# Optimization experiments

Hardware: AMD Instinct MI355X
Metric: run time of the kernel (lower is better)

## Reference

```python
import jax, jax.numpy as jnp
import numpy as np

N_STREAMS = 4096


def setup_inputs() -> dict:
    key = jax.random.key(0)
    # Plain Gaussian (well-separated singular values; the polar factor math is
    # identical to the module's eye + 0.01*randn init, just a different point).
    H_raw = jax.random.normal(key, (N_STREAMS, N_STREAMS), dtype=jnp.float32)
    return {"H_raw": H_raw}


def reference(H_raw) -> jnp.ndarray:
    # OrthogonalMixing.forward: orthogonal polar factor of H_raw via thin SVD.
    U, s, Vh = jnp.linalg.svd(H_raw, full_matrices=False)
    return U @ Vh  # (s, s), satisfies H^T H = I
```

## Files before the change

kernel.cpp:

```cpp
#include <hip/hip_runtime.h>
#include <hip/hip_bf16.h>

#define NN 4096
#define NITER 12
#define NGROW 9
#define NPOW 12

using bf16 = __hip_bfloat16;
typedef __attribute__((ext_vector_type(4))) float f32x4;
typedef __attribute__((ext_vector_type(8))) short s16x8;
typedef __attribute__((ext_vector_type(8))) unsigned short u16x8;

__device__ inline float bf2f(unsigned short u) {
  union { unsigned int i; float f; } c; c.i = ((unsigned int)u) << 16; return c.f;
}
__device__ inline unsigned short f2bf(float f) {
  bf16 t = (bf16)f; return *(unsigned short*)&t;
}

__device__ inline void gl_lds16(const void* g, void* l) {
  __builtin_amdgcn_global_load_lds(
      (const __attribute__((address_space(1))) unsigned int*)(unsigned long long)(uintptr_t)g,
      (__attribute__((address_space(3))) unsigned int*)(uintptr_t)l,
      16, 0, 0);
}

template <int EPI, int TRI>
__global__ __launch_bounds__(256, 2) void gemm_nt(
    const bf16* __restrict__ P, const bf16* __restrict__ Q,
    void* __restrict__ Out, const bf16* __restrict__ aux,
    float alpha, float beta) {
  if (TRI && blockIdx.y > blockIdx.x) return;
  __shared__ bf16 lp[128 * 64];
  __shared__ bf16 lq[128 * 64];

  const int tid = threadIdx.x;
  const int lane = tid & 63;
  const int wv = tid >> 6;
  const int wr = wv >> 1, wc = wv & 1;
  const int bi = blockIdx.x, bj = blockIdx.y;

  const int m = lane & 15;
  const int qd = lane >> 4;
  const int lrow = lane >> 3;
  const int lchunk = lane & 7;

  f32x4 acc[4][4] = {};

  for (int k0 = 0; k0 < NN; k0 += 64) {
    __syncthreads();
#pragma unroll
    for (int s = 0; s < 4; ++s) {
      const int t = wv * 4 + s;
      const int r = t * 8 + lrow;
      const int gc = lchunk ^ (r & 7);
      const bf16* gp = P + (size_t)(bi * 128 + r) * NN + k0 + gc * 8;
      gl_lds16(gp, &lp[t * 512 + lane * 8]);
      const bf16* gq = Q + (size_t)(bj * 128 + r) * NN + k0 + gc * 8;
      gl_lds16(gq, &lq[t * 512 + lane * 8]);
    }
    __syncthreads();

#pragma unroll
    for (int sub = 0; sub < 2; ++sub) {
      s16x8 av[4], bv[4];
#pragma unroll
      for (int f = 0; f < 4; ++f) {
        const int ra = wr * 64 + f * 16 + m;
        const int ca = (sub * 4 + qd) ^ (ra & 7);
        av[f] = *(const s16x8*)&lp[ra * 64 + ca * 8];
        const int rb = wc * 64 + f * 16 + m;
        const int cb = (sub * 4 + qd) ^ (rb & 7);
        bv[f] = *(const s16x8*)&lq[rb * 64 + cb * 8];
      }
#pragma unroll
      for (int fr = 0; fr < 4; ++fr)
#pragma unroll
        for (int fc = 0; fc < 4; ++fc)
          acc[fr][fc] = __builtin_amdgcn_mfma_f32_16x16x32_bf16(
              av[fr], bv[fc], acc[fr][fc], 0, 0, 0);
    }
  }

#pragma unroll
  for (int fr = 0; fr < 4; ++fr) {
#pragma unroll
    for (int fc = 0; fc < 4; ++fc) {
#pragma unroll
      for (int rg = 0; rg < 4; ++rg) {
        const int grow = bi * 128 + wr * 64 + fr * 16 + qd * 4 + rg;
        const int gcol = bj * 128 + wc * 64 + fc * 16 + m;
        const size_t idx = (size_t)grow * NN + gcol;
        float v = beta * acc[fr][fc][rg];
        if (alpha != 0.0f) v += alpha * (float)aux[idx];
        if (EPI == 0)
          ((bf16*)Out)[idx] = (bf16)v;
        else
          ((float*)Out)[idx] = v;
      }
    }
  }
}

__global__ void transpose_bf16(const bf16* __restrict__ in, bf16* __restrict__ out) {
  __shared__ bf16 tile[64][65];
  const int tx = threadIdx.x & 63;
  const int ty = threadIdx.x >> 6;
  const int bx = blockIdx.x, by = blockIdx.y;
#pragma unroll
  for (int rr = 0; rr < 16; ++rr) {
    const int row = rr * 4 + ty;
    tile[row][tx] = in[(size_t)(by * 64 + row) * NN + bx * 64 + tx];
  }
  __syncthreads();
#pragma unroll
  for (int rr = 0; rr < 16; ++rr) {
    const int row = rr * 4 + ty;
    out[(size_t)(bx * 64 + row) * NN + by * 64 + tx] = tile[tx][row];
  }
}

__global__ void mirror_upper(bf16* __restrict__ A) {
  const int bx = blockIdx.x, by = blockIdx.y;
  if (by <= bx) return;
  __shared__ bf16 tile[64][65];
  const int tx = threadIdx.x & 63;
  const int ty = threadIdx.x >> 6;
#pragma unroll
  for (int rr = 0; rr < 16; ++rr) {
    const int row = rr * 4 + ty;
    tile[row][tx] = A[(size_t)(by * 64 + row) * NN + bx * 64 + tx];
  }
  __syncthreads();
#pragma unroll
  for (int rr = 0; rr < 16; ++rr) {
    const int row = rr * 4 + ty;
    A[(size_t)(bx * 64 + row) * NN + by * 64 + tx] = tile[tx][row];
  }
}

__global__ __launch_bounds__(256) void powmv(const bf16* __restrict__ A,
                                             const float* __restrict__ vin,
                                             const float* __restrict__ snin,
                                             float* __restrict__ vout,
                                             float* __restrict__ snout) {
  const float scale = rsqrtf(*snin);
  const int row = blockIdx.x * 4 + (threadIdx.x >> 6);
  const int lane = threadIdx.x & 63;
  const unsigned short* arow = (const unsigned short*)A + (size_t)row * NN;
  float acc = 0.0f;
#pragma unroll
  for (int p = 0; p < 8; ++p) {
    const int c = p * 512 + lane * 8;
    const u16x8 av = *(const u16x8*)(arow + c);
    const float4 w0 = *(const float4*)(vin + c);
    const float4 w1 = *(const float4*)(vin + c + 4);
    acc += bf2f(av[0]) * w0.x + bf2f(av[1]) * w0.y + bf2f(av[2]) * w0.z +
           bf2f(av[3]) * w0.w + bf2f(av[4]) * w1.x + bf2f(av[5]) * w1.y +
           bf2f(av[6]) * w1.z + bf2f(av[7]) * w1.w;
  }
  for (int off = 32; off; off >>= 1) acc += __shfl_down(acc, off, 64);
  if (lane == 0) {
    const float u = acc * scale;
    vout[row] = u;
    atomicAdd(snout, u * u);
  }
}

__global__ void init_pw(float* __restrict__ v0, float* __restrict__ slots) {
  const int t = threadIdx.x;
  if (t < 64) slots[t] = (t == 1) ? 1.0f : 0.0f;
  for (int i = t; i < NN; i += 256) {
    const unsigned h = (unsigned)i * 2654435761u;
    v0[i] = ((h >> 16) & 1) ? 0.015625f : -0.015625f;
  }
}

__global__ void reduce_sumsq(const float* __restrict__ h, float* __restrict__ slots) {
  float acc = 0.0f;
  const size_t total = (size_t)NN * NN;
  for (size_t i = (size_t)blockIdx.x * blockDim.x + threadIdx.x; i < total;
       i += (size_t)gridDim.x * blockDim.x) {
    const float v = h[i];
    acc += v * v;
  }
  for (int off = 32; off; off >>= 1) acc += __shfl_down(acc, off, 64);
  __shared__ float ws[4];
  const int lane = threadIdx.x & 63, wv = threadIdx.x >> 6;
  if (lane == 0) ws[wv] = acc;
  __syncthreads();
  if (threadIdx.x == 0) atomicAdd(&slots[0], ws[0] + ws[1] + ws[2] + ws[3]);
}

__global__ void scale_cast(const float* __restrict__ h, const float* __restrict__ slots,
                           bf16* __restrict__ xb, int mode) {
  float inv = rsqrtf(slots[0]);
  if (mode) inv *= rsqrtf(1.10f * sqrtf(slots[1 + NPOW]));
  const size_t i = ((size_t)blockIdx.x * blockDim.x + threadIdx.x) * 4;
  const float4 v = *(const float4*)(h + i);
  union { bf16 b[4]; ushort4 u; } cvt;
  cvt.b[0] = (bf16)(v.x * inv);
  cvt.b[1] = (bf16)(v.y * inv);
  cvt.b[2] = (bf16)(v.z * inv);
  cvt.b[3] = (bf16)(v.w * inv);
  *(ushort4*)(xb + i) = cvt.u;
}

__global__ void rescale_bf16(bf16* __restrict__ a, const float* __restrict__ slots) {
  const float cA = 1.0f / (1.10f * sqrtf(slots[1 + NPOW]));
  const size_t i = ((size_t)blockIdx.x * 256 + threadIdx.x) * 8;
  unsigned short* p = (unsigned short*)a + i;
  u16x8 v = *(u16x8*)p;
  u16x8 o;
#pragma unroll
  for (int j = 0; j < 8; ++j) o[j] = f2bf(bf2f(v[j]) * cA);
  *(u16x8*)p = o;
}

extern "C" void kernel_launch(void* const* d_in, const int* in_sizes, int n_in,
                              void* d_out, int out_size, void* d_ws, size_t ws_size,
                              hipStream_t stream) {
  (void)in_sizes; (void)n_in; (void)out_size; (void)ws_size;
  const float* H = (const float*)d_in[0];
  float* out = (float*)d_out;
  char* ws = (char*)d_ws;

  bf16* P0 = (bf16*)ws;
  bf16* P1 = (bf16*)(ws + ((size_t)32 << 20));
  bf16* Ab = (bf16*)(ws + ((size_t)64 << 20));
  bf16* Bb = (bf16*)((char*)d_out + ((size_t)32 << 20));
  float* v0 = (float*)d_out;
  float* v1 = (float*)((char*)d_out + 16384);
  float* slots = (float*)((char*)d_out + 32768);

  const dim3 g(32, 32), tb(256), gt(64, 64);

  init_pw<<<1, 256, 0, stream>>>(v0, slots);
  reduce_sumsq<<<1024, 256, 0, stream>>>(H, slots);
  scale_cast<<<(NN * (size_t)NN) / 4 / 256, 256, 0, stream>>>(H, slots, P0, 0);
  transpose_bf16<<<gt, tb, 0, stream>>>(P0, P1);
  gemm_nt<0, 1><<<g, tb, 0, stream>>>(P1, P1, Ab, (bf16*)nullptr, 0.0f, 1.0f);
  mirror_upper<<<gt, tb, 0, stream>>>(Ab);
  for (int k = 0; k < NPOW; ++k) {
    const float* vi = (k & 1) ? v1 : v0;
    float* vo = (k & 1) ? v0 : v1;
    powmv<<<1024, 256, 0, stream>>>(Ab, vi, &slots[1 + k], vo, &slots[2 + k]);
  }
  rescale_bf16<<<(NN * (size_t)NN) / 8 / 256, 256, 0, stream>>>(Ab, slots);
  scale_cast<<<(NN * (size_t)NN) / 4 / 256, 256, 0, stream>>>(H, slots, P0, 1);

  bf16* X = P0;
  bf16* Y = P1;
  const float GA = 3.4445f, GB = -4.7750f, GC = 2.0315f;
  const float PA = 1.875f, PB = -1.25f, PC = 0.375f;

  for (int it = 0; it < NITER; ++it) {
    const bool polish = it >= NGROW;
    const bool last = (it == NITER - 1);
    const float qa = polish ? PA : GA, qb = polish ? PB : GB, qc = polish ? PC : GC;

    if (it > 0) {
      transpose_bf16<<<gt, tb, 0, stream>>>(X, Y);
      gemm_nt<0, 1><<<g, tb, 0, stream>>>(Y, Y, Ab, (bf16*)nullptr, 0.0f, 1.0f);
      mirror_upper<<<gt, tb, 0, stream>>>(Ab);
    }
    bf16* Bdst = last ? Y : Bb;
    gemm_nt<0, 1><<<g, tb, 0, stream>>>(Ab, Ab, Bdst, Ab, qb, qc);
    mirror_upper<<<gt, tb, 0, stream>>>(Bdst);
    if (!last) {
      gemm_nt<0, 0><<<g, tb, 0, stream>>>(X, Bdst, Y, X, qa, 1.0f);
      bf16* t = X; X = Y; Y = t;
    } else {
      gemm_nt<1, 0><<<g, tb, 0, stream>>>(X, Bdst, out, X, qa, 1.0f);
    }
  }
}
```

Measured before the change: 5.321 ms.

## Switch polar iteration to fp16, packed triangular grid, fused mirroring, fewer iterations

Moves every matrix and the MFMA path from bf16 to fp16, with a prescale of 32 on X so values keep fp16 precision. Launches only the 528 lower-triangle tiles through a triangular index map and writes the mirrored tile from the GEMM epilogue, which removes the separate mirror kernels and the early-exit blocks. Cuts the Newton-Schulz schedule from 12 iterations to 10 (8 growth, 2 polish) and raises the launch-bounds occupancy hint. The fewer polish steps and the fp16 range both put accuracy at risk, and the scattered transposed stores in the epilogue are uncoalesced.

```diff
diff --git a/kernel.cpp b/kernel.cpp
--- a/kernel.cpp
+++ b/kernel.cpp
@@ -1,22 +1,18 @@
 #include <hip/hip_runtime.h>
 #include <hip/hip_bf16.h>
+#include <hip/hip_fp16.h>
 
 #define NN 4096
-#define NITER 12
-#define NGROW 9
+#define NGROW 8
+#define NPOL 2
+#define NITER (NGROW + NPOL)
 #define NPOW 12
-
-using bf16 = __hip_bfloat16;
+#define NTRI 528
+#define PRESCALE 32.0f
+
+using f16 = _Float16;
 typedef __attribute__((ext_vector_type(4))) float f32x4;
-typedef __attribute__((ext_vector_type(8))) short s16x8;
-typedef __attribute__((ext_vector_type(8))) unsigned short u16x8;
-
-__device__ inline float bf2f(unsigned short u) {
-  union { unsigned int i; float f; } c; c.i = ((unsigned int)u) << 16; return c.f;
-}
-__device__ inline unsigned short f2bf(float f) {
-  bf16 t = (bf16)f; return *(unsigned short*)&t;
-}
+typedef __attribute__((ext_vector_type(8))) f16 h16x8;
 
 __device__ inline void gl_lds16(const void* g, void* l) {
   __builtin_amdgcn_global_load_lds(
@@ -26,19 +22,30 @@
 }
 
 template <int EPI, int TRI>
-__global__ __launch_bounds__(256, 2) void gemm_nt(
-    const bf16* __restrict__ P, const bf16* __restrict__ Q,
-    void* __restrict__ Out, const bf16* __restrict__ aux,
+__global__ __launch_bounds__(256, 4) void gemm_nt(
+    const f16* __restrict__ P, const f16* __restrict__ Q,
+    void* __restrict__ Out, const f16* __restrict__ aux,
     float alpha, float beta) {
-  if (TRI && blockIdx.y > blockIdx.x) return;
-  __shared__ bf16 lp[128 * 64];
-  __shared__ bf16 lq[128 * 64];
+  int bi, bj;
+  if (TRI) {
+    const int t = blockIdx.x;
+    int r = (int)((sqrtf(8.0f * (float)t + 1.0f) - 1.0f) * 0.5f);
+    while ((r + 1) * (r + 2) / 2 <= t) ++r;
+    while (r * (r + 1) / 2 > t) --r;
+    bi = r;
+    bj = t - r * (r + 1) / 2;
+  } else {
+    bi = blockIdx.x;
+    bj = blockIdx.y;
+  }
+
+  __shared__ f16 lp[128 * 64];
+  __shared__ f16 lq[128 * 64];
 
   const int tid = threadIdx.x;
   const int lane = tid & 63;
   const int wv = tid >> 6;
   const int wr = wv >> 1, wc = wv & 1;
-  const int bi = blockIdx.x, bj = blockIdx.y;
 
   const int m = lane & 15;
   const int qd = lane >> 4;
@@ -54,30 +61,30 @@
       const int t = wv * 4 + s;
       const int r = t * 8 + lrow;
       const int gc = lchunk ^ (r & 7);
-      const bf16* gp = P + (size_t)(bi * 128 + r) * NN + k0 + gc * 8;
+      const f16* gp = P + (size_t)(bi * 128 + r) * NN + k0 + gc * 8;
       gl_lds16(gp, &lp[t * 512 + lane * 8]);
-      const bf16* gq = Q + (size_t)(bj * 128 + r) * NN + k0 + gc * 8;
+      const f16* gq = Q + (size_t)(bj * 128 + r) * NN + k0 + gc * 8;
       gl_lds16(gq, &lq[t * 512 + lane * 8]);
     }
     __syncthreads();
 
 #pragma unroll
     for (int sub = 0; sub < 2; ++sub) {
-      s16x8 av[4], bv[4];
+      h16x8 av[4], bv[4];
 #pragma unroll
       for (int f = 0; f < 4; ++f) {
         const int ra = wr * 64 + f * 16 + m;
         const int ca = (sub * 4 + qd) ^ (ra & 7);
-        av[f] = *(const s16x8*)&lp[ra * 64 + ca * 8];
+        av[f] = *(const h16x8*)&lp[ra * 64 + ca * 8];
         const int rb = wc * 64 + f * 16 + m;
         const int cb = (sub * 4 + qd) ^ (rb & 7);
-        bv[f] = *(const s16x8*)&lq[rb * 64 + cb * 8];
+        bv[f] = *(const h16x8*)&lq[rb * 64 + cb * 8];
       }
 #pragma unroll
       for (int fr = 0; fr < 4; ++fr)
 #pragma unroll
         for (int fc = 0; fc < 4; ++fc)
-          acc[fr][fc] = __builtin_amdgcn_mfma_f32_16x16x32_bf16(
+          acc[fr][fc] = __builtin_amdgcn_mfma_f32_16x16x32_f16(
               av[fr], bv[fc], acc[fr][fc], 0, 0, 0);
     }
   }
@@ -88,22 +95,27 @@
     for (int fc = 0; fc < 4; ++fc) {
 #pragma unroll
       for (int rg = 0; rg < 4; ++rg) {
-        const int grow = bi * 128 + wr * 64 + fr * 16 + qd * 4 + rg;
-        const int gcol = bj * 128 + wc * 64 + fc * 16 + m;
-        const size_t idx = (size_t)grow * NN + gcol;
+        const int lr = wr * 64 + fr * 16 + qd * 4 + rg;
+        const int lc = wc * 64 + fc * 16 + m;
+        const size_t idx = (size_t)(bi * 128 + lr) * NN + bj * 128 + lc;
         float v = beta * acc[fr][fc][rg];
         if (alpha != 0.0f) v += alpha * (float)aux[idx];
         if (EPI == 0)
-          ((bf16*)Out)[idx] = (bf16)v;
+          ((f16*)Out)[idx] = (f16)v;
         else
           ((float*)Out)[idx] = v;
+        if (TRI && bi != bj) {
+          const size_t idxT = (size_t)(bj * 128 + lc) * NN + bi * 128 + lr;
+          ((f16*)Out)[idxT] = (f16)v;
+        }
       }
     }
   }
 }
 
-__global__ void transpose_bf16(const bf16* __restrict__ in, bf16* __restrict__ out) {
-  __shared__ bf16 tile[64][65];
+__global__ void transpose_h(const unsigned short* __restrict__ in,
+                            unsigned short* __restrict__ out) {
+  __shared__ unsigned short tile[64][65];
   const int tx = threadIdx.x & 63;
   const int ty = threadIdx.x >> 6;
   const int bx = blockIdx.x, by = blockIdx.y;
@@ -120,26 +132,7 @@
   }
 }
 
-__global__ void mirror_upper(bf16* __restrict__ A) {
-  const int bx = blockIdx.x, by = blockIdx.y;
-  if (by <= bx) return;
-  __shared__ bf16 tile[64][65];
-  const int tx = threadIdx.x & 63;
-  const int ty = threadIdx.x >> 6;
-#pragma unroll
-  for (int rr = 0; rr < 16; ++rr) {
-    const int row = rr * 4 + ty;
-    tile[row][tx] = A[(size_t)(by * 64 + row) * NN + bx * 64 + tx];
-  }
-  __syncthreads();
-#pragma unroll
-  for (int rr = 0; rr < 16; ++rr) {
-    const int row = rr * 4 + ty;
-    A[(size_t)(bx * 64 + row) * NN + by * 64 + tx] = tile[tx][row];
-  }
-}
-
-__global__ __launch_bounds__(256) void powmv(const bf16* __restrict__ A,
+__global__ __launch_bounds__(256) void powmv(const f16* __restrict__ A,
                                              const float* __restrict__ vin,
                                              const float* __restrict__ snin,
                                              float* __restrict__ vout,
@@ -147,17 +140,17 @@
   const float scale = rsqrtf(*snin);
   const int row = blockIdx.x * 4 + (threadIdx.x >> 6);
   const int lane = threadIdx.x & 63;
-  const unsigned short* arow = (const unsigned short*)A + (size_t)row * NN;
+  const f16* arow = A + (size_t)row * NN;
   float acc = 0.0f;
 #pragma unroll
   for (int p = 0; p < 8; ++p) {
     const int c = p * 512 + lane * 8;
-    const u16x8 av = *(const u16x8*)(arow + c);
+    const h16x8 av = *(const h16x8*)(arow + c);
     const float4 w0 = *(const float4*)(vin + c);
     const float4 w1 = *(const float4*)(vin + c + 4);
-    acc += bf2f(av[0]) * w0.x + bf2f(av[1]) * w0.y + bf2f(av[2]) * w0.z +
-           bf2f(av[3]) * w0.w + bf2f(av[4]) * w1.x + bf2f(av[5]) * w1.y +
-           bf2f(av[6]) * w1.z + bf2f(av[7]) * w1.w;
+    acc += (float)av[0] * w0.x + (float)av[1] * w0.y + (float)av[2] * w0.z +
+           (float)av[3] * w0.w + (float)av[4] * w1.x + (float)av[5] * w1.y +
+           (float)av[6] * w1.z + (float)av[7] * w1.w;
   }
   for (int off = 32; off; off >>= 1) acc += __shfl_down(acc, off, 64);
   if (lane == 0) {
@@ -193,28 +186,27 @@
 }
 
 __global__ void scale_cast(const float* __restrict__ h, const float* __restrict__ slots,
-                           bf16* __restrict__ xb, int mode) {
-  float inv = rsqrtf(slots[0]);
+                           f16* __restrict__ xb, int mode) {
+  float inv = rsqrtf(slots[0]) * PRESCALE;
   if (mode) inv *= rsqrtf(1.10f * sqrtf(slots[1 + NPOW]));
   const size_t i = ((size_t)blockIdx.x * blockDim.x + threadIdx.x) * 4;
   const float4 v = *(const float4*)(h + i);
-  union { bf16 b[4]; ushort4 u; } cvt;
-  cvt.b[0] = (bf16)(v.x * inv);
-  cvt.b[1] = (bf16)(v.y * inv);
-  cvt.b[2] = (bf16)(v.z * inv);
-  cvt.b[3] = (bf16)(v.w * inv);
+  union { f16 hh[4]; ushort4 u; } cvt;
+  cvt.hh[0] = (f16)(v.x * inv);
+  cvt.hh[1] = (f16)(v.y * inv);
+  cvt.hh[2] = (f16)(v.z * inv);
+  cvt.hh[3] = (f16)(v.w * inv);
   *(ushort4*)(xb + i) = cvt.u;
 }
 
-__global__ void rescale_bf16(bf16* __restrict__ a, const float* __restrict__ slots) {
+__global__ void rescale_f16(f16* __restrict__ a, const float* __restrict__ slots) {
   const float cA = 1.0f / (1.10f * sqrtf(slots[1 + NPOW]));
   const size_t i = ((size_t)blockIdx.x * 256 + threadIdx.x) * 8;
-  unsigned short* p = (unsigned short*)a + i;
-  u16x8 v = *(u16x8*)p;
-  u16x8 o;
-#pragma unroll
-  for (int j = 0; j < 8; ++j) o[j] = f2bf(bf2f(v[j]) * cA);
-  *(u16x8*)p = o;
+  h16x8 v = *(h16x8*)(a + i);
+  h16x8 o;
+#pragma unroll
+  for (int j = 0; j < 8; ++j) o[j] = (f16)((float)v[j] * cA);
+  *(h16x8*)(a + i) = o;
 }
 
 extern "C" void kernel_launch(void* const* d_in, const int* in_sizes, int n_in,
@@ -225,32 +217,31 @@
   float* out = (float*)d_out;
   char* ws = (char*)d_ws;
 
-  bf16* P0 = (bf16*)ws;
-  bf16* P1 = (bf16*)(ws + ((size_t)32 << 20));
-  bf16* Ab = (bf16*)(ws + ((size_t)64 << 20));
-  bf16* Bb = (bf16*)((char*)d_out + ((size_t)32 << 20));
+  f16* P0 = (f16*)ws;
+  f16* P1 = (f16*)(ws + ((size_t)32 << 20));
+  f16* Ab = (f16*)(ws + ((size_t)64 << 20));
+  f16* Bb = (f16*)((char*)d_out + ((size_t)32 << 20));
   float* v0 = (float*)d_out;
   float* v1 = (float*)((char*)d_out + 16384);
   float* slots = (float*)((char*)d_out + 32768);
 
-  const dim3 g(32, 32), tb(256), gt(64, 64);
+  const dim3 gfull(32, 32), tb(256), gt(64, 64);
 
   init_pw<<<1, 256, 0, stream>>>(v0, slots);
   reduce_sumsq<<<1024, 256, 0, stream>>>(H, slots);
   scale_cast<<<(NN * (size_t)NN) / 4 / 256, 256, 0, stream>>>(H, slots, P0, 0);
-  transpose_bf16<<<gt, tb, 0, stream>>>(P0, P1);
-  gemm_nt<0, 1><<<g, tb, 0, stream>>>(P1, P1, Ab, (bf16*)nullptr, 0.0f, 1.0f);
-  mirror_upper<<<gt, tb, 0, stream>>>(Ab);
+  transpose_h<<<gt, tb, 0, stream>>>((const unsigned short*)P0, (unsigned short*)P1);
+  gemm_nt<0, 1><<<NTRI, tb, 0, stream>>>(P1, P1, Ab, (f16*)nullptr, 0.0f, 1.0f);
   for (int k = 0; k < NPOW; ++k) {
     const float* vi = (k & 1) ? v1 : v0;
     float* vo = (k & 1) ? v0 : v1;
     powmv<<<1024, 256, 0, stream>>>(Ab, vi, &slots[1 + k], vo, &slots[2 + k]);
   }
-  rescale_bf16<<<(NN * (size_t)NN) / 8 / 256, 256, 0, stream>>>(Ab, slots);
+  rescale_f16<<<(NN * (size_t)NN) / 8 / 256, 256, 0, stream>>>(Ab, slots);
   scale_cast<<<(NN * (size_t)NN) / 4 / 256, 256, 0, stream>>>(H, slots, P0, 1);
 
-  bf16* X = P0;
-  bf16* Y = P1;
+  f16* X = P0;
+  f16* Y = P1;
   const float GA = 3.4445f, GB = -4.7750f, GC = 2.0315f;
   const float PA = 1.875f, PB = -1.25f, PC = 0.375f;
 
@@ -260,18 +251,16 @@
     const float qa = polish ? PA : GA, qb = polish ? PB : GB, qc = polish ? PC : GC;
 
     if (it > 0) {
-      transpose_bf16<<<gt, tb, 0, stream>>>(X, Y);
-      gemm_nt<0, 1><<<g, tb, 0, stream>>>(Y, Y, Ab, (bf16*)nullptr, 0.0f, 1.0f);
-      mirror_upper<<<gt, tb, 0, stream>>>(Ab);
-    }
-    bf16* Bdst = last ? Y : Bb;
-    gemm_nt<0, 1><<<g, tb, 0, stream>>>(Ab, Ab, Bdst, Ab, qb, qc);
-    mirror_upper<<<gt, tb, 0, stream>>>(Bdst);
+      transpose_h<<<gt, tb, 0, stream>>>((const unsigned short*)X, (unsigned short*)Y);
+      gemm_nt<0, 1><<<NTRI, tb, 0, stream>>>(Y, Y, Ab, (f16*)nullptr, 0.0f, 1.0f);
+    }
+    f16* Bdst = last ? Y : Bb;
+    gemm_nt<0, 1><<<NTRI, tb, 0, stream>>>(Ab, Ab, Bdst, Ab, qb, qc);
     if (!last) {
-      gemm_nt<0, 0><<<g, tb, 0, stream>>>(X, Bdst, Y, X, qa, 1.0f);
-      bf16* t = X; X = Y; Y = t;
+      gemm_nt<0, 0><<<gfull, tb, 0, stream>>>(X, Bdst, Y, X, qa, 1.0f);
+      f16* t = X; X = Y; Y = t;
     } else {
-      gemm_nt<1, 0><<<g, tb, 0, stream>>>(X, Bdst, out, X, qa, 1.0f);
-    }
-  }
-}
+      gemm_nt<1, 0><<<gfull, tb, 0, stream>>>(X, Bdst, out, X, qa, 1.0f);
+    }
+  }
+}
```

Result: faster. 4.586 ms (-13.8%).
